# Optimization experiments

Hardware: AMD Instinct MI355X
Metric: run time of the kernel (lower is better)

## Reference

```python
import jax, jax.numpy as jnp
import numpy as np

EMB_DIM = 300
VOCAB_X = 50000
VOCAB_Y = 50000
LEN_X = 64
LEN_Y = 64
BATCH = 1024
PAD_ID = 0


def setup_inputs() -> dict:
    key = jax.random.key(0)
    k1, k2, k3, k4, k5, k6, k7 = jax.random.split(key, 7)
    initrange = 0.5 / EMB_DIM
    emb_x = jax.random.uniform(k1, (VOCAB_X, EMB_DIM), jnp.float32, -initrange, initrange)
    emb_y = jax.random.uniform(k2, (VOCAB_Y, EMB_DIM), jnp.float32, -initrange, initrange)
    # padding row zeroed as in init_emb
    emb_x = emb_x.at[PAD_ID].set(0.0)
    emb_y = emb_y.at[PAD_ID].set(0.0)
    return {
        "samp_hid": jax.random.normal(k3, (BATCH, EMB_DIM), jnp.float32),
        "batch_x": jax.random.randint(k4, (BATCH, LEN_X), 0, VOCAB_X, jnp.int64 if jax.config.jax_enable_x64 else jnp.int32),
        "batch_y": jax.random.randint(k5, (BATCH, LEN_Y), 0, VOCAB_Y, jnp.int64 if jax.config.jax_enable_x64 else jnp.int32),
        "emb_x": emb_x,
        "emb_y": emb_y,
        "bias_x": jax.random.uniform(k6, (VOCAB_X,), jnp.float32),
        "bias_y": jax.random.uniform(k7, (VOCAB_Y,), jnp.float32),
    }


def _cal_nll(z, tokens, emb, bias):
    # logits shared across all positions: [B, V]
    logits = z @ emb.T + bias
    logp = jax.nn.log_softmax(logits, axis=-1)            # compute log-softmax ONCE per row
    tok_logp = jnp.take_along_axis(logp, tokens, axis=1)  # [B, L] gather per-position targets
    mask = (tokens != PAD_ID).astype(logits.dtype)        # CrossEntropyLoss(ignore_index=0)
    return jnp.sum(-tok_logp * mask, axis=1)              # sum over positions -> [B]


def reference(samp_hid, batch_x, batch_y, emb_x, emb_y, bias_x, bias_y):
    nll_x = _cal_nll(samp_hid, batch_x, emb_x, bias_x)
    nll_y = _cal_nll(samp_hid, batch_y, emb_y, bias_y)
    return jnp.mean(nll_x + nll_y)
```

## Files before the change

kernel.cpp:

```cpp
#include <hip/hip_runtime.h>

#define V_VOCAB 50000
#define K_DIM   300
#define NROWS   1024
#define LEN     64
#define NBC     392
#define CGS     784
#define KS      19
#define PASSES  32
#define LOG2E   1.44269504088896f

typedef __attribute__((ext_vector_type(8)))  short bf16x8;
typedef __attribute__((ext_vector_type(16))) float f32x16;

static __device__ __forceinline__ unsigned short f2bf(float f) {
    unsigned int u = __builtin_bit_cast(unsigned int, f);
    u = u + 0x7fffu + ((u >> 16) & 1u);
    return (unsigned short)(u >> 16);
}

static __device__ __forceinline__ f32x16 zero16() {
    f32x16 z;
#pragma unroll
    for (int i = 0; i < 16; ++i) z[i] = 0.0f;
    return z;
}

static __device__ __forceinline__ void gload_lds16(const void* g, void* l) {
    __builtin_amdgcn_global_load_lds((const __attribute__((address_space(1))) void*)g,
                                     (__attribute__((address_space(3))) void*)l, 16, 0, 0);
}

__global__ void zbf_kernel(const float* __restrict__ z, unsigned short* __restrict__ zbf) {
    int t = blockIdx.x * 256 + threadIdx.x;
    int l    = t & 63;
    int rest = t >> 6;
    int ks   = rest % KS;
    int rblk = rest / KS;
    int row  = rblk * 32 + (l & 31);
    int k0   = ks * 16 + (l >> 5) * 8;
    unsigned short o[8];
#pragma unroll
    for (int j = 0; j < 8; ++j) {
        int k = k0 + j;
        float v = (k < K_DIM) ? z[row * K_DIM + k] * LOG2E
                              : ((k == K_DIM) ? LOG2E : 0.0f);
        o[j] = f2bf(v);
    }
    ushort4* p = (ushort4*)(zbf + (size_t)t * 8);
    p[0] = make_ushort4(o[0], o[1], o[2], o[3]);
    p[1] = make_ushort4(o[4], o[5], o[6], o[7]);
}

__attribute__((amdgpu_waves_per_eu(2, 2)))
__global__ void __launch_bounds__(128)
gemm_kernel(const unsigned short* __restrict__ zbf,
            const float* __restrict__ emb_x,
            const float* __restrict__ emb_y,
            const float* __restrict__ bias_x,
            const float* __restrict__ bias_y,
            float* __restrict__ partial,
            float* __restrict__ lsesum,
            int accmode) {
    __shared__ unsigned short Zs[2][9728];

    const int tid  = threadIdx.x;
    const int lane = tid & 63;
    const int w    = tid >> 6;
    const int side = blockIdx.y;
    const int bc   = blockIdx.x;
    const float* eg = side ? emb_y : emb_x;
    const float* bg = side ? bias_y : bias_x;

    {
        const unsigned short* src = zbf;
#pragma unroll
        for (int i = 0; i < 10; ++i) {
            int q = w * 10 + i;
            if (q > 18) q = 18;
            gload_lds16(src + (size_t)q * 512 + lane * 8, &Zs[0][q * 512]);
        }
    }

    bf16x8 a0[KS], a1[KS];
#pragma unroll
    for (int cb = 0; cb < 2; ++cb) {
        const int c  = bc * 128 + w * 64 + cb * 32 + (lane & 31);
        const bool cv = (c < V_VOCAB);
        const float* erow = eg + (size_t)c * K_DIM;
        const int khi = (lane >> 5) * 8;
#pragma unroll
        for (int ks = 0; ks < KS; ++ks) {
            const int k0 = ks * 16 + khi;
            float f[8];
            if (k0 + 8 <= K_DIM) {
                float4 u  = cv ? *(const float4*)(erow + k0)     : make_float4(0, 0, 0, 0);
                float4 v2 = cv ? *(const float4*)(erow + k0 + 4) : make_float4(0, 0, 0, 0);
                f[0] = u.x;  f[1] = u.y;  f[2] = u.z;  f[3] = u.w;
                f[4] = v2.x; f[5] = v2.y; f[6] = v2.z; f[7] = v2.w;
            } else {
#pragma unroll
                for (int j = 0; j < 8; ++j) {
                    int k = k0 + j;
                    f[j] = (k < K_DIM) ? (cv ? erow[k] : 0.0f)
                         : (k == K_DIM ? (cv ? bg[c] : -3e38f) : 0.0f);
                }
            }
            bf16x8 t;
#pragma unroll
            for (int j = 0; j < 8; ++j) t[j] = (short)f2bf(f[j]);
            if (cb == 0) a0[ks] = t; else a1[ks] = t;
        }
    }

    float* pout = partial + ((size_t)side * CGS + (size_t)bc * 2 + w) * NROWS;
    float* lout = lsesum + side * NROWS;

    int buf = 0;
    for (int p = 0; p < PASSES; ++p) {
        if (p < PASSES - 1) {
            const unsigned short* src = zbf + (size_t)(p + 1) * 9728;
#pragma unroll
            for (int i = 0; i < 10; ++i) {
                int q = w * 10 + i;
                if (q > 18) q = 18;
                gload_lds16(src + (size_t)q * 512 + lane * 8, &Zs[buf ^ 1][q * 512]);
            }
            asm volatile("s_waitcnt vmcnt(10)" ::: "memory");
        } else {
            asm volatile("s_waitcnt vmcnt(0)" ::: "memory");
        }
        __builtin_amdgcn_s_barrier();
        __builtin_amdgcn_sched_barrier(0);

        const unsigned short* zb = &Zs[buf][0];
        f32x16 acc0 = zero16(), acc1 = zero16();
#pragma unroll
        for (int ks = 0; ks < KS; ++ks) {
            bf16x8 b = *(const bf16x8*)(zb + ((size_t)ks * 64 + lane) * 8);
            acc0 = __builtin_amdgcn_mfma_f32_32x32x16_bf16(a0[ks], b, acc0, 0, 0, 0);
            acc1 = __builtin_amdgcn_mfma_f32_32x32x16_bf16(a1[ks], b, acc1, 0, 0, 0);
        }

        float s0 = 0.0f, s1 = 0.0f;
#pragma unroll
        for (int r = 0; r < 16; ++r) {
            s0 += exp2f(acc0[r]);
            s1 += exp2f(acc1[r]);
        }
        float t = s0 + s1;
        t += __shfl_xor(t, 32, 64);
        if (accmode) { if (lane < 32) atomicAdd(lout + p * 32 + lane, t); }
        else         { if (lane < 32) pout[p * 32 + lane] = t; }

        __builtin_amdgcn_s_barrier();
        buf ^= 1;
    }
}

__global__ void lse_kernel(const float* __restrict__ partial, float* __restrict__ lse) {
    __shared__ float red[1024];
    int side = blockIdx.x >> 4;
    int mg   = blockIdx.x & 15;
    int m    = mg * 64 + (threadIdx.x & 63);
    int sg   = threadIdx.x >> 6;
    const float* p = partial + (size_t)side * CGS * NROWS;
    float s = 0.0f;
    for (int cg = sg; cg < CGS; cg += 16)
        s += p[(size_t)cg * NROWS + m];
    red[threadIdx.x] = s;
    __syncthreads();
    if (threadIdx.x < 64) {
        float t = 0.0f;
#pragma unroll
        for (int j = 0; j < 16; ++j) t += red[threadIdx.x + 64 * j];
        lse[side * NROWS + mg * 64 + threadIdx.x] = logf(t);
    }
}

__global__ void lse_log_kernel(float* __restrict__ lsesum) {
    int g = blockIdx.x * 1024 + threadIdx.x;
    if (g < 2 * NROWS) lsesum[g] = logf(lsesum[g]);
}

__global__ void gatherdot_kernel(const float* __restrict__ z,
                                 const int* __restrict__ tok_x, const int* __restrict__ tok_y,
                                 const float* __restrict__ emb_x, const float* __restrict__ emb_y,
                                 const float* __restrict__ bias_x, const float* __restrict__ bias_y,
                                 const float* __restrict__ lse, float* __restrict__ nllpart) {
    __shared__ float gs[304];
    const int b = blockIdx.x, side = blockIdx.y, tid = threadIdx.x;
    const int* tokp = (side ? tok_y : tok_x) + b * LEN;
    const float* eg = side ? emb_y : emb_x;
    if (tid < K_DIM) {
        float g0 = 0.0f, g1 = 0.0f, g2 = 0.0f, g3 = 0.0f;
#pragma unroll 4
        for (int pos = 0; pos < LEN; pos += 4) {
            int t0 = tokp[pos], t1 = tokp[pos + 1], t2 = tokp[pos + 2], t3 = tokp[pos + 3];
            if (t0) g0 += eg[(size_t)t0 * K_DIM + tid];
            if (t1) g1 += eg[(size_t)t1 * K_DIM + tid];
            if (t2) g2 += eg[(size_t)t2 * K_DIM + tid];
            if (t3) g3 += eg[(size_t)t3 * K_DIM + tid];
        }
        gs[tid] = (g0 + g1) + (g2 + g3);
    }
    __syncthreads();
    if (tid < 64) {
        const float* bg = side ? bias_y : bias_x;
        float dp = 0.0f;
#pragma unroll
        for (int i = 0; i < 5; ++i) {
            int d = tid + i * 64;
            if (d < K_DIM) dp += z[(size_t)b * K_DIM + d] * gs[d];
        }
        int t = tokp[tid];
        float bs = t ? bg[t] : 0.0f;
        float ct = t ? 1.0f : 0.0f;
#pragma unroll
        for (int off = 32; off > 0; off >>= 1) {
            dp += __shfl_xor(dp, off, 64);
            bs += __shfl_xor(bs, off, 64);
            ct += __shfl_xor(ct, off, 64);
        }
        if (tid == 0) nllpart[side * NROWS + b] = ct * lse[side * NROWS + b] - dp - bs;
    }
}

__global__ void finalize_kernel(const float* __restrict__ nllpart, float* __restrict__ out) {
    __shared__ float r16[16];
    int i = threadIdx.x;
    float v = nllpart[i] + nllpart[NROWS + i];
#pragma unroll
    for (int off = 32; off > 0; off >>= 1) v += __shfl_xor(v, off, 64);
    if ((i & 63) == 0) r16[i >> 6] = v;
    __syncthreads();
    if (i < 64) {
        float x = (i < 16) ? r16[i] : 0.0f;
#pragma unroll
        for (int off = 8; off > 0; off >>= 1) x += __shfl_xor(x, off, 64);
        if (i == 0) out[0] = x * (1.0f / 1024.0f);
    }
}

extern "C" void kernel_launch(void* const* d_in, const int* in_sizes, int n_in,
                              void* d_out, int out_size, void* d_ws, size_t ws_size,
                              hipStream_t stream) {
    const float* z      = (const float*)d_in[0];
    const int*   tok_x  = (const int*)d_in[1];
    const int*   tok_y  = (const int*)d_in[2];
    const float* emb_x  = (const float*)d_in[3];
    const float* emb_y  = (const float*)d_in[4];
    const float* bias_x = (const float*)d_in[5];
    const float* bias_y = (const float*)d_in[6];
    float* out = (float*)d_out;

    char* ws = (char*)d_ws;
    const size_t ZBF_B  = 622592;
    const size_t PART_B = (size_t)2 * CGS * NROWS * 4;
    const size_t need   = ZBF_B + PART_B + 8192 + 8192;

    unsigned short* zbf = (unsigned short*)ws;
    zbf_kernel<<<152, 256, 0, stream>>>(z, zbf);

    if (ws_size >= need) {
        float* partial = (float*)(ws + ZBF_B);
        float* lse     = (float*)(ws + ZBF_B + PART_B);
        float* nllpart = (float*)(ws + ZBF_B + PART_B + 8192);
        gemm_kernel<<<dim3(NBC, 2), 128, 0, stream>>>(zbf, emb_x, emb_y, bias_x, bias_y,
                                                      partial, lse , 0);
        lse_kernel<<<32, 1024, 0, stream>>>(partial, lse);
        gatherdot_kernel<<<dim3(NROWS, 2), 320, 0, stream>>>(z, tok_x, tok_y, emb_x, emb_y,
                                                             bias_x, bias_y, lse, nllpart);
        finalize_kernel<<<1, 1024, 0, stream>>>(nllpart, out);
    } else {
        float* lse     = (float*)(ws + ZBF_B);
        float* nllpart = (float*)(ws + ZBF_B + 8192);
        hipMemsetAsync(lse, 0, 8192, stream);
        gemm_kernel<<<dim3(NBC, 2), 128, 0, stream>>>(zbf, emb_x, emb_y, bias_x, bias_y,
                                                      nllpart , lse, 1);
        lse_log_kernel<<<2, 1024, 0, stream>>>(lse);
        gatherdot_kernel<<<dim3(NROWS, 2), 320, 0, stream>>>(z, tok_x, tok_y, emb_x, emb_y,
                                                             bias_x, bias_y, lse, nllpart);
        finalize_kernel<<<1, 1024, 0, stream>>>(nllpart, out);
    }
}
```

Measured before the change: 186.1 us.

## Give each wave its own 32-column vocab slice and split gatherdot by halves

The GEMM kernel drops the LDS double-buffered staging of the bf16 hidden matrix. Each wave now owns one 32-column vocabulary slice and reads B fragments straight from global memory, launching twice as many waves to raise occupancy and remove the per-pass barriers. This multiplies L2 read traffic for the shared hidden matrix and doubles the partial-sum buffer that lse_kernel must reduce. Separately, gatherdot splits each row's 64 tokens into two halves for more blocks, and finalize sums the two partials.

```diff
diff --git a/kernel.cpp b/kernel.cpp
--- a/kernel.cpp
+++ b/kernel.cpp
@@ -4,10 +4,9 @@
 #define K_DIM   300
 #define NROWS   1024
 #define LEN     64
-#define NBC     392
-#define CGS     784
+#define NCG     1564
 #define KS      19
-#define PASSES  32
+#define RBLK    32
 #define LOG2E   1.44269504088896f
 
 typedef __attribute__((ext_vector_type(8)))  short bf16x8;
@@ -24,11 +23,6 @@
 #pragma unroll
     for (int i = 0; i < 16; ++i) z[i] = 0.0f;
     return z;
-}
-
-static __device__ __forceinline__ void gload_lds16(const void* g, void* l) {
-    __builtin_amdgcn_global_load_lds((const __attribute__((address_space(1))) void*)g,
-                                     (__attribute__((address_space(3))) void*)l, 16, 0, 0);
 }
 
 __global__ void zbf_kernel(const float* __restrict__ z, unsigned short* __restrict__ zbf) {
@@ -52,8 +46,7 @@
     p[1] = make_ushort4(o[4], o[5], o[6], o[7]);
 }
 
-__attribute__((amdgpu_waves_per_eu(2, 2)))
-__global__ void __launch_bounds__(128)
+__global__ void __launch_bounds__(256, 4)
 gemm_kernel(const unsigned short* __restrict__ zbf,
             const float* __restrict__ emb_x,
             const float* __restrict__ emb_y,
@@ -62,30 +55,17 @@
             float* __restrict__ partial,
             float* __restrict__ lsesum,
             int accmode) {
-    __shared__ unsigned short Zs[2][9728];
-
     const int tid  = threadIdx.x;
     const int lane = tid & 63;
-    const int w    = tid >> 6;
-    const int side = blockIdx.y;
-    const int bc   = blockIdx.x;
+    const int wid  = blockIdx.x * 4 + (tid >> 6);
+    const int side = (wid >= NCG) ? 1 : 0;
+    const int cg   = wid - side * NCG;
     const float* eg = side ? emb_y : emb_x;
     const float* bg = side ? bias_y : bias_x;
 
+    bf16x8 a[KS];
     {
-        const unsigned short* src = zbf;
-#pragma unroll
-        for (int i = 0; i < 10; ++i) {
-            int q = w * 10 + i;
-            if (q > 18) q = 18;
-            gload_lds16(src + (size_t)q * 512 + lane * 8, &Zs[0][q * 512]);
-        }
-    }
-
-    bf16x8 a0[KS], a1[KS];
-#pragma unroll
-    for (int cb = 0; cb < 2; ++cb) {
-        const int c  = bc * 128 + w * 64 + cb * 32 + (lane & 31);
+        const int c  = cg * 32 + (lane & 31);
         const bool cv = (c < V_VOCAB);
         const float* erow = eg + (size_t)c * K_DIM;
         const int khi = (lane >> 5) * 8;
@@ -109,52 +89,29 @@
             bf16x8 t;
 #pragma unroll
             for (int j = 0; j < 8; ++j) t[j] = (short)f2bf(f[j]);
-            if (cb == 0) a0[ks] = t; else a1[ks] = t;
-        }
-    }
-
-    float* pout = partial + ((size_t)side * CGS + (size_t)bc * 2 + w) * NROWS;
+            a[ks] = t;
+        }
+    }
+
+    float* pout = partial + (size_t)wid * NROWS;
     float* lout = lsesum + side * NROWS;
 
-    int buf = 0;
-    for (int p = 0; p < PASSES; ++p) {
-        if (p < PASSES - 1) {
-            const unsigned short* src = zbf + (size_t)(p + 1) * 9728;
-#pragma unroll
-            for (int i = 0; i < 10; ++i) {
-                int q = w * 10 + i;
-                if (q > 18) q = 18;
-                gload_lds16(src + (size_t)q * 512 + lane * 8, &Zs[buf ^ 1][q * 512]);
-            }
-            asm volatile("s_waitcnt vmcnt(10)" ::: "memory");
-        } else {
-            asm volatile("s_waitcnt vmcnt(0)" ::: "memory");
-        }
-        __builtin_amdgcn_s_barrier();
-        __builtin_amdgcn_sched_barrier(0);
-
-        const unsigned short* zb = &Zs[buf][0];
-        f32x16 acc0 = zero16(), acc1 = zero16();
+    for (int rb = 0; rb < RBLK; ++rb) {
+        const bf16x8* bp = (const bf16x8*)(zbf + (size_t)rb * KS * 512);
+        f32x16 acc = zero16();
 #pragma unroll
         for (int ks = 0; ks < KS; ++ks) {
-            bf16x8 b = *(const bf16x8*)(zb + ((size_t)ks * 64 + lane) * 8);
-            acc0 = __builtin_amdgcn_mfma_f32_32x32x16_bf16(a0[ks], b, acc0, 0, 0, 0);
-            acc1 = __builtin_amdgcn_mfma_f32_32x32x16_bf16(a1[ks], b, acc1, 0, 0, 0);
-        }
-
-        float s0 = 0.0f, s1 = 0.0f;
-#pragma unroll
-        for (int r = 0; r < 16; ++r) {
-            s0 += exp2f(acc0[r]);
-            s1 += exp2f(acc1[r]);
-        }
-        float t = s0 + s1;
-        t += __shfl_xor(t, 32, 64);
-        if (accmode) { if (lane < 32) atomicAdd(lout + p * 32 + lane, t); }
-        else         { if (lane < 32) pout[p * 32 + lane] = t; }
-
-        __builtin_amdgcn_s_barrier();
-        buf ^= 1;
+            bf16x8 b = bp[ks * 64 + lane];
+            acc = __builtin_amdgcn_mfma_f32_32x32x16_bf16(a[ks], b, acc, 0, 0, 0);
+        }
+        float s = 0.0f;
+#pragma unroll
+        for (int r = 0; r < 16; ++r) s += exp2f(acc[r]);
+        s += __shfl_xor(s, 32, 64);
+        if (accmode) { if (lane < 32) atomicAdd(lout + rb * 32 + lane, s); }
+        else         { if (lane < 32) pout[rb * 32 + lane] = s; }
+
+        if ((rb & 3) == 3) __builtin_amdgcn_s_barrier();
     }
 }
 
@@ -164,9 +121,9 @@
     int mg   = blockIdx.x & 15;
     int m    = mg * 64 + (threadIdx.x & 63);
     int sg   = threadIdx.x >> 6;
-    const float* p = partial + (size_t)side * CGS * NROWS;
+    const float* p = partial + (size_t)side * NCG * NROWS;
     float s = 0.0f;
-    for (int cg = sg; cg < CGS; cg += 16)
+    for (int cg = sg; cg < NCG; cg += 16)
         s += p[(size_t)cg * NROWS + m];
     red[threadIdx.x] = s;
     __syncthreads();
@@ -187,15 +144,16 @@
                                  const int* __restrict__ tok_x, const int* __restrict__ tok_y,
                                  const float* __restrict__ emb_x, const float* __restrict__ emb_y,
                                  const float* __restrict__ bias_x, const float* __restrict__ bias_y,
-                                 const float* __restrict__ lse, float* __restrict__ nllpart) {
+                                 const float* __restrict__ lse, float* __restrict__ gdpart) {
     __shared__ float gs[304];
-    const int b = blockIdx.x, side = blockIdx.y, tid = threadIdx.x;
-    const int* tokp = (side ? tok_y : tok_x) + b * LEN;
+    const int b = blockIdx.x, side = blockIdx.y & 1, half = blockIdx.y >> 1;
+    const int tid = threadIdx.x;
+    const int* tokp = (side ? tok_y : tok_x) + b * LEN + half * 32;
     const float* eg = side ? emb_y : emb_x;
     if (tid < K_DIM) {
         float g0 = 0.0f, g1 = 0.0f, g2 = 0.0f, g3 = 0.0f;
 #pragma unroll 4
-        for (int pos = 0; pos < LEN; pos += 4) {
+        for (int pos = 0; pos < 32; pos += 4) {
             int t0 = tokp[pos], t1 = tokp[pos + 1], t2 = tokp[pos + 2], t3 = tokp[pos + 3];
             if (t0) g0 += eg[(size_t)t0 * K_DIM + tid];
             if (t1) g1 += eg[(size_t)t1 * K_DIM + tid];
@@ -213,7 +171,7 @@
             int d = tid + i * 64;
             if (d < K_DIM) dp += z[(size_t)b * K_DIM + d] * gs[d];
         }
-        int t = tokp[tid];
+        int t = (tid < 32) ? tokp[tid] : 0;
         float bs = t ? bg[t] : 0.0f;
         float ct = t ? 1.0f : 0.0f;
 #pragma unroll
@@ -222,14 +180,17 @@
             bs += __shfl_xor(bs, off, 64);
             ct += __shfl_xor(ct, off, 64);
         }
-        if (tid == 0) nllpart[side * NROWS + b] = ct * lse[side * NROWS + b] - dp - bs;
-    }
-}
-
-__global__ void finalize_kernel(const float* __restrict__ nllpart, float* __restrict__ out) {
+        if (tid == 0)
+            gdpart[((size_t)side * NROWS + b) * 2 + half] =
+                ct * lse[side * NROWS + b] - dp - bs;
+    }
+}
+
+__global__ void finalize_kernel(const float* __restrict__ gdpart, float* __restrict__ out) {
     __shared__ float r16[16];
     int i = threadIdx.x;
-    float v = nllpart[i] + nllpart[NROWS + i];
+    float v = gdpart[i * 2] + gdpart[i * 2 + 1]
+            + gdpart[(NROWS + i) * 2] + gdpart[(NROWS + i) * 2 + 1];
 #pragma unroll
     for (int off = 32; off > 0; off >>= 1) v += __shfl_xor(v, off, 64);
     if ((i & 63) == 0) r16[i >> 6] = v;
@@ -256,8 +217,8 @@
 
     char* ws = (char*)d_ws;
     const size_t ZBF_B  = 622592;
-    const size_t PART_B = (size_t)2 * CGS * NROWS * 4;
-    const size_t need   = ZBF_B + PART_B + 8192 + 8192;
+    const size_t PART_B = (size_t)2 * NCG * NROWS * 4;
+    const size_t need   = ZBF_B + PART_B + 8192 + 16384;
 
     unsigned short* zbf = (unsigned short*)ws;
     zbf_kernel<<<152, 256, 0, stream>>>(z, zbf);
@@ -265,22 +226,22 @@
     if (ws_size >= need) {
         float* partial = (float*)(ws + ZBF_B);
         float* lse     = (float*)(ws + ZBF_B + PART_B);
-        float* nllpart = (float*)(ws + ZBF_B + PART_B + 8192);
-        gemm_kernel<<<dim3(NBC, 2), 128, 0, stream>>>(zbf, emb_x, emb_y, bias_x, bias_y,
-                                                      partial, lse , 0);
+        float* gdpart  = (float*)(ws + ZBF_B + PART_B + 8192);
+        gemm_kernel<<<782, 256, 0, stream>>>(zbf, emb_x, emb_y, bias_x, bias_y,
+                                             partial, lse , 0);
         lse_kernel<<<32, 1024, 0, stream>>>(partial, lse);
-        gatherdot_kernel<<<dim3(NROWS, 2), 320, 0, stream>>>(z, tok_x, tok_y, emb_x, emb_y,
-                                                             bias_x, bias_y, lse, nllpart);
-        finalize_kernel<<<1, 1024, 0, stream>>>(nllpart, out);
+        gatherdot_kernel<<<dim3(NROWS, 4), 320, 0, stream>>>(z, tok_x, tok_y, emb_x, emb_y,
+                                                             bias_x, bias_y, lse, gdpart);
+        finalize_kernel<<<1, 1024, 0, stream>>>(gdpart, out);
     } else {
-        float* lse     = (float*)(ws + ZBF_B);
-        float* nllpart = (float*)(ws + ZBF_B + 8192);
+        float* lse    = (float*)(ws + ZBF_B);
+        float* gdpart = (float*)(ws + ZBF_B + 8192);
         hipMemsetAsync(lse, 0, 8192, stream);
-        gemm_kernel<<<dim3(NBC, 2), 128, 0, stream>>>(zbf, emb_x, emb_y, bias_x, bias_y,
-                                                      nllpart , lse, 1);
+        gemm_kernel<<<782, 256, 0, stream>>>(zbf, emb_x, emb_y, bias_x, bias_y,
+                                             gdpart , lse, 1);
         lse_log_kernel<<<2, 1024, 0, stream>>>(lse);
-        gatherdot_kernel<<<dim3(NROWS, 2), 320, 0, stream>>>(z, tok_x, tok_y, emb_x, emb_y,
-                                                             bias_x, bias_y, lse, nllpart);
-        finalize_kernel<<<1, 1024, 0, stream>>>(nllpart, out);
-    }
-}
+        gatherdot_kernel<<<dim3(NROWS, 4), 320, 0, stream>>>(z, tok_x, tok_y, emb_x, emb_y,
+                                                             bias_x, bias_y, lse, gdpart);
+        finalize_kernel<<<1, 1024, 0, stream>>>(gdpart, out);
+    }
+}
```

Measured after the change: 226.8 us. +21.9%, slower.
